# Performance work log

Measured on AMD Instinct MI355X. Metric: run time of the kernel, lower is better.

## Reference

```python
import jax, jax.numpy as jnp
import numpy as np

P, N, E, H = 8192, 32, 256, 8
D = E // H
CUT_A, CUT_B = 0.001, 0.005  # self.length_range = (0.001, 0.005, None, None)
SQRT3 = 1.7320508075688772


def _soft_square_cutoff(x):
    # smooth ramp 0->1 on [CUT_A, CUT_B], 0 below, 1 above (high-side ranges are None)
    t = jnp.clip((x - CUT_A) / (CUT_B - CUT_A), 0.0, 1.0)
    return 0.5 * (1.0 - jnp.cos(jnp.pi * t))


def setup_inputs() -> dict:
    key = jax.random.key(0)
    ks = jax.random.split(key, 16)
    s = 1.0 / np.sqrt(E)
    inp = {
        "query": jax.random.normal(ks[0], (P, E), jnp.float32),
        "key_x": jax.random.normal(ks[1], (P, E), jnp.float32),
        "value": jax.random.normal(ks[2], (P, E), jnp.float32),
        "index_pair": jax.random.randint(ks[3], (P, N), 0, P),
        "relative_atten_weights": jax.random.normal(ks[4], (P, N, H), jnp.float32),
        # lengths ~ N(0, 0.002*sqrt(3)) so they span the (0.001, 0.005) cutoff range
        "rpe_distance": jax.random.normal(ks[5], (P, N, 3), jnp.float32) * 0.002,
        "Wq": jax.random.normal(ks[6], (E, E), jnp.float32) * s,
        "bq": jnp.zeros((E,), jnp.float32),
        "Wk": jax.random.normal(ks[7], (E, E), jnp.float32) * s,
        "bk": jnp.zeros((E,), jnp.float32),
        "Wv": jax.random.normal(ks[8], (E, E), jnp.float32) * s,
        "bv": jnp.zeros((E,), jnp.float32),
        "Wg1": jax.random.normal(ks[9], (E, 3 * H), jnp.float32) * s,
        "bg1": jnp.zeros((3 * H,), jnp.float32),
        "Wg2": jax.random.normal(ks[10], (3 * H, 3 * H), jnp.float32) * (1.0 / np.sqrt(3 * H)),
        "bg2": jnp.zeros((3 * H,), jnp.float32),
    }
    return inp


def reference(query, key_x, value, index_pair, relative_atten_weights, rpe_distance,
              Wq, bq, Wk, bk, Wv, bv, Wg1, bg1, Wg2, bg2):
    # --- RPE spherical harmonics (irreps 1x0e+1x1e, component norm); keep l=1 part ([:,1:])
    rlen = jnp.linalg.norm(rpe_distance, axis=-1, keepdims=True)        # [P,N,1]
    unit = rpe_distance / jnp.maximum(rlen, 1e-12)                      # normalize=True
    cutoff = _soft_square_cutoff(rlen)                                  # nonscalar cutoff
    rpe_edge_sh = SQRT3 * unit * cutoff                                 # [P,N,3]

    # --- projections
    q = query @ Wq + bq                                                 # [P,E]
    k = key_x @ Wk + bk
    v = value @ Wv + bv

    # --- mapper_v6: per-edge gather of key/value rows
    k_g = k[index_pair]                                                 # [P,N,E]
    v_g = v[index_pair]                                                 # [P,N,E]

    # --- dot-product attention logits
    qh = q.reshape(P, H, D)
    kh = k_g.reshape(P, N, H, D)
    dot_atten = jnp.einsum('phd,pnhd->pnh', qh, kh)                     # [P,N,H]

    # --- MLP positional bias gated by spherical harmonics
    diff = k_g - q[:, None, :]                                          # [P,N,E]
    g = jax.nn.relu(diff @ Wg1 + bg1) @ Wg2 + bg2                       # [P,N,3H]
    g = g.reshape(P, N, H, 3)
    pos_atten = jnp.sum(g * rpe_edge_sh[:, :, None, :], axis=-1)        # [P,N,H]

    atten = (dot_atten + pos_atten + relative_atten_weights) / np.sqrt(D)
    atten = jax.nn.softmax(atten, axis=1)                               # over neighbors

    vh = v_g.reshape(P, N, H, D)
    out = jnp.einsum('pnh,pnhc->phc', atten, vh).reshape(P, E)
    return out
```

## Files before the change

kernel.cpp:

```cpp
#include <hip/hip_runtime.h>
#include <stdint.h>

typedef uint32_t u32;
typedef unsigned short u16;

#define LDT 40

typedef __bf16 bf16x8 __attribute__((ext_vector_type(8)));
typedef float  f32x4  __attribute__((ext_vector_type(4)));
typedef _Float16 h16x2 __attribute__((ext_vector_type(2)));
typedef u32    u32x4  __attribute__((ext_vector_type(4)));
typedef u32    u32x2  __attribute__((ext_vector_type(2)));
typedef float  f32x4v __attribute__((ext_vector_type(4)));

__device__ __forceinline__ float bf2f(u16 x) {
  union { float f; u32 u; } c; c.u = ((u32)x) << 16; return c.f;
}
__device__ __forceinline__ u16 f2bf(float f) {
  union { float f; u32 u; } c; c.f = f;
  u32 b = c.u;
  return (u16)((b + 0x7FFFu + ((b >> 16) & 1u)) >> 16);
}
__device__ __forceinline__ u32 pk2(float lo, float hi) {
  return (u32)f2bf(lo) | ((u32)f2bf(hi) << 16);
}
__device__ __forceinline__ u16 f2h(float f) {
  union { _Float16 h; u16 u; } c; c.h = (_Float16)f; return c.u;
}
__device__ __forceinline__ float h2f(u16 x) {
  union { _Float16 h; u16 u; } c; c.u = x; return (float)c.h;
}
__device__ __forceinline__ u32 h2bf2(u32 w) {
  return pk2(h2f((u16)(w & 0xFFFF)), h2f((u16)(w >> 16)));
}
__device__ __forceinline__ float fdot2u(u32 a, u32 b, float c) {
  union { u32 u; h16x2 h; } ua, ub; ua.u = a; ub.u = b;
#if __has_builtin(__builtin_amdgcn_fdot2)
  return __builtin_amdgcn_fdot2(ua.h, ub.h, c, false);
#else
  return c + (float)ua.h.x * (float)ub.h.x + (float)ua.h.y * (float)ub.h.y;
#endif
}

__global__ __launch_bounds__(256) void prep_transpose(
    const float* __restrict__ Wq, const float* __restrict__ Wk, const float* __restrict__ Wv,
    const float* __restrict__ Wg2, const float* __restrict__ Wg1,
    u16* __restrict__ WTq, u16* __restrict__ WTk, u16* __restrict__ WTv,
    u16* __restrict__ wg2bf, u16* __restrict__ wg1T)
{
  int z = blockIdx.z, bx = blockIdx.x, by = blockIdx.y;
  int x = threadIdx.x, y = threadIdx.y;
  if (z == 3) {
    if (bx || by) return;
    int t = y * 32 + x;
    for (int i = t; i < 1280; i += 256) {
      int j = i / 40, k = i % 40;
      float v = (j < 24 && k < 24) ? Wg2[(size_t)k * 24 + j] : 0.f;
      wg2bf[i] = f2bf(v);
    }
    for (int j = 0; j < 24; j++)
      wg1T[(size_t)j * 256 + t] = f2bf(Wg1[(size_t)t * 24 + j]);
    for (int j = 24; j < 32; j++)
      wg1T[(size_t)j * 256 + t] = 0;
    return;
  }
  __shared__ u16 tile[32][33];
  const float* W  = (z == 0) ? Wq : (z == 1) ? Wk : Wv;
  u16*         WT = (z == 0) ? WTq : (z == 1) ? WTk : WTv;
  for (int yy = y; yy < 32; yy += 8)
    tile[yy][x] = f2bf(W[(size_t)(by * 32 + yy) * 256 + bx * 32 + x]);
  __syncthreads();
  for (int yy = y; yy < 32; yy += 8)
    WT[(size_t)(bx * 32 + yy) * 256 + by * 32 + x] = tile[x][yy];
}

__global__ __launch_bounds__(256) void gemm_qkv(
    const float* __restrict__ Xq, const float* __restrict__ Xk, const float* __restrict__ Xv,
    const u16* __restrict__ WTq, const u16* __restrict__ WTk, const u16* __restrict__ WTv,
    const float* __restrict__ bq, const float* __restrict__ bk, const float* __restrict__ bv,
    u16* __restrict__ Oq, u16* __restrict__ Ok, u16* __restrict__ Ov)
{
  int z = blockIdx.z;
  const float* X    = (z == 0) ? Xq : (z == 1) ? Xk : Xv;
  const u16*   WT   = (z == 0) ? WTq : (z == 1) ? WTk : WTv;
  const float* bias = (z == 0) ? bq : (z == 1) ? bk : bv;
  u16*         O    = (z == 0) ? Oq : (z == 1) ? Ok : Ov;

  int m0 = blockIdx.x * 64;
  int n0 = blockIdx.y * 128;
  int t = threadIdx.x;
  int lane = t & 63, wid = t >> 6;
  int wr = wid >> 1, wc = wid & 1;
  int fr = lane & 15, fg = lane >> 4;
  int sra = t >> 2;
  int sca = (t & 3) * 8;
  int srb = t >> 1;
  int scb = (t & 1) * 16;

  __shared__ __align__(16) u16 la[64 * LDT];
  __shared__ __align__(16) u16 lb[128 * LDT];

  f32x4 acc[2][4];
#pragma unroll
  for (int i = 0; i < 2; i++)
#pragma unroll
    for (int j = 0; j < 4; j++) acc[i][j] = (f32x4){0.f, 0.f, 0.f, 0.f};

  for (int kt = 0; kt < 256; kt += 32) {
    const float4* ga = (const float4*)(X + (size_t)(m0 + sra) * 256 + kt + sca);
    float4 a0 = ga[0], a1 = ga[1];
    const uint4* gb = (const uint4*)(WT + (size_t)(n0 + srb) * 256 + kt + scb);
    uint4 b0 = gb[0], b1 = gb[1];

    uint4 wa;
    wa.x = pk2(a0.x, a0.y); wa.y = pk2(a0.z, a0.w);
    wa.z = pk2(a1.x, a1.y); wa.w = pk2(a1.z, a1.w);

    __syncthreads();
    *(uint4*)&la[sra * LDT + sca]     = wa;
    *(uint4*)&lb[srb * LDT + scb]     = b0;
    *(uint4*)&lb[srb * LDT + scb + 8] = b1;
    __syncthreads();

    bf16x8 af[2], bfr[4];
#pragma unroll
    for (int s = 0; s < 2; s++)
      af[s] = *(const bf16x8*)&la[(wr * 32 + s * 16 + fr) * LDT + fg * 8];
#pragma unroll
    for (int j = 0; j < 4; j++)
      bfr[j] = *(const bf16x8*)&lb[(wc * 64 + j * 16 + fr) * LDT + fg * 8];
#pragma unroll
    for (int i = 0; i < 2; i++)
#pragma unroll
      for (int j = 0; j < 4; j++)
        acc[i][j] = __builtin_amdgcn_mfma_f32_16x16x32_bf16(af[i], bfr[j], acc[i][j], 0, 0, 0);
  }

#pragma unroll
  for (int i = 0; i < 2; i++) {
    int rowb = m0 + wr * 32 + i * 16 + fg * 4;
#pragma unroll
    for (int j = 0; j < 4; j++) {
      int col = n0 + wc * 64 + j * 16 + fr;
      float bb = bias[col];
#pragma unroll
      for (int r = 0; r < 4; r++)
        O[(size_t)(rowb + r) * 256 + col] = f2h(acc[i][j][r] + bb);
    }
  }
}

__global__ __launch_bounds__(256) void gemm_g1(
    const u16* __restrict__ kbuf, const u16* __restrict__ qbuf,
    const u16* __restrict__ wg1T, const float* __restrict__ bg1,
    u16* __restrict__ kg1, u16* __restrict__ qadj)
{
  int z = blockIdx.y;
  const u16* X = (z == 0) ? kbuf : qbuf;
  u16*       O = (z == 0) ? kg1 : qadj;

  int m0 = blockIdx.x * 128;
  int t = threadIdx.x;
  int lane = t & 63, wid = t >> 6;
  int fr = lane & 15, fg = lane >> 4;
  int sr = t >> 1;
  int sc = (t & 1) * 16;

  __shared__ __align__(16) u16 la[128 * LDT];
  __shared__ __align__(16) u16 lb[32 * LDT];

  f32x4 acc[2][2];
#pragma unroll
  for (int i = 0; i < 2; i++)
#pragma unroll
    for (int j = 0; j < 2; j++) acc[i][j] = (f32x4){0.f, 0.f, 0.f, 0.f};

  for (int kt = 0; kt < 256; kt += 32) {
    const uint4* ga = (const uint4*)(X + (size_t)(m0 + sr) * 256 + kt + sc);
    uint4 a0 = ga[0], a1 = ga[1];
    uint4 b0, b1;
    if (t < 64) {
      const uint4* gb = (const uint4*)(wg1T + (size_t)sr * 256 + kt + sc);
      b0 = gb[0]; b1 = gb[1];
    }
    uint4 wa0, wa1;
    wa0.x = h2bf2(a0.x); wa0.y = h2bf2(a0.y);
    wa0.z = h2bf2(a0.z); wa0.w = h2bf2(a0.w);
    wa1.x = h2bf2(a1.x); wa1.y = h2bf2(a1.y);
    wa1.z = h2bf2(a1.z); wa1.w = h2bf2(a1.w);

    __syncthreads();
    *(uint4*)&la[sr * LDT + sc]     = wa0;
    *(uint4*)&la[sr * LDT + sc + 8] = wa1;
    if (t < 64) {
      *(uint4*)&lb[sr * LDT + sc]     = b0;
      *(uint4*)&lb[sr * LDT + sc + 8] = b1;
    }
    __syncthreads();

    bf16x8 af[2], bfr[2];
#pragma unroll
    for (int s = 0; s < 2; s++)
      af[s] = *(const bf16x8*)&la[(wid * 32 + s * 16 + fr) * LDT + fg * 8];
#pragma unroll
    for (int s = 0; s < 2; s++)
      bfr[s] = *(const bf16x8*)&lb[(s * 16 + fr) * LDT + fg * 8];
#pragma unroll
    for (int i = 0; i < 2; i++)
#pragma unroll
      for (int j = 0; j < 2; j++)
        acc[i][j] = __builtin_amdgcn_mfma_f32_16x16x32_bf16(af[i], bfr[j], acc[i][j], 0, 0, 0);
  }

#pragma unroll
  for (int i = 0; i < 2; i++) {
    int rowb = m0 + wid * 32 + i * 16 + fg * 4;
#pragma unroll
    for (int j = 0; j < 2; j++) {
      int col = j * 16 + fr;
      if (col < 24) {
        float sub = (z == 1) ? bg1[col] : 0.f;
#pragma unroll
        for (int r = 0; r < 4; r++)
          O[(size_t)(rowb + r) * 32 + col] = f2h(acc[i][j][r] - sub);
      }
    }
  }
}

__global__ __launch_bounds__(256) void attn_logits(
    const u16* __restrict__ qb, const u16* __restrict__ kb,
    const u16* __restrict__ kg1g, const u16* __restrict__ qadjg,
    const int* __restrict__ ip, const float* __restrict__ raw,
    const float* __restrict__ rpe, const u16* __restrict__ wg2bf,
    const float* __restrict__ bg2g, u16* __restrict__ attg)
{
  int p = blockIdx.x, t = threadIdx.x;
  int lane = t & 63, w = t >> 6;
  int fr = lane & 15, fg = lane >> 4;
  int n = t >> 3, h = t & 7;

  __shared__ __align__(16) u16   wg2_s[32 * 40];
  __shared__ __align__(16) u16   kg1_s[32 * 40];
  __shared__              float qadj_s[24];
  __shared__              float bg2_s[24];
  __shared__              float sh_s[96];
  __shared__              float g_s[32 * 33];
  __shared__              float ev_s[256];
  __shared__              float is_s[8];

  int myidx = ip[(size_t)p * 32 + n];

  uint4 kg1w = {0, 0, 0, 0};
  if ((t & 7) < 4) kg1w = *(const uint4*)(kg1g + (size_t)myidx * 32 + (t & 7) * 8);
  uint4 wgw = {0, 0, 0, 0};
  if (t < 160) wgw = ((const uint4*)wg2bf)[t];
  float rx = 0.f, ry = 0.f, rz = 0.f;
  if (t >= 160 && t < 192) {
    int nn = t - 160;
    rx = __builtin_nontemporal_load(rpe + (size_t)p * 96 + nn * 3 + 0);
    ry = __builtin_nontemporal_load(rpe + (size_t)p * 96 + nn * 3 + 1);
    rz = __builtin_nontemporal_load(rpe + (size_t)p * 96 + nn * 3 + 2);
  }
  u16 qaw = 0;
  if (t >= 192 && t < 216)
    qaw = __builtin_nontemporal_load(qadjg + (size_t)p * 32 + (t - 192));
  float bgw = 0.f;
  if (t >= 224 && t < 248) bgw = bg2g[t - 224];

  const uint4* kr = (const uint4*)(kb + (size_t)myidx * 256 + h * 32);
  uint4 k0 = kr[0], k1 = kr[1], k2 = kr[2], k3 = kr[3];
  const u32x4* qr = (const u32x4*)(qb + (size_t)p * 256 + h * 32);
  u32x4 q0 = __builtin_nontemporal_load(qr + 0);
  u32x4 q1 = __builtin_nontemporal_load(qr + 1);
  u32x4 q2 = __builtin_nontemporal_load(qr + 2);
  u32x4 q3 = __builtin_nontemporal_load(qr + 3);
  float rw = __builtin_nontemporal_load(raw + (size_t)p * 256 + t);

  if ((t & 7) < 4) *(uint4*)&kg1_s[n * 40 + (t & 7) * 8] = kg1w;
  if (t < 160) *(uint4*)&wg2_s[t * 8] = wgw;
  else if (t < 192) {
    int nn = t - 160;
    float rl = sqrtf(rx * rx + ry * ry + rz * rz);
    float inv = 1.f / fmaxf(rl, 1e-12f);
    float tt2 = fminf(fmaxf((rl - 0.001f) * 250.f, 0.f), 1.f);
    float cut = 0.5f * (1.f - cosf(tt2 * 3.14159265358979f));
    float s3c = 1.7320508075688772f * inv * cut;
    sh_s[nn * 3 + 0] = rx * s3c; sh_s[nn * 3 + 1] = ry * s3c; sh_s[nn * 3 + 2] = rz * s3c;
  }
  else if (t >= 192 && t < 216) qadj_s[t - 192] = h2f(qaw);
  else if (t >= 224 && t < 248) bg2_s[t - 224] = bgw;
  __syncthreads();

  {
    int mt = w & 1, jt = w >> 1;
    union { u32 u[4]; bf16x8 v; } a;
    if (fg < 3) {
      const u16*   krow = &kg1_s[(mt * 16 + fr) * 40 + fg * 8];
      const float* qrow = &qadj_s[fg * 8];
      float x0 = fmaxf(h2f(krow[0]) - qrow[0], 0.f), x1 = fmaxf(h2f(krow[1]) - qrow[1], 0.f);
      float x2 = fmaxf(h2f(krow[2]) - qrow[2], 0.f), x3 = fmaxf(h2f(krow[3]) - qrow[3], 0.f);
      float x4 = fmaxf(h2f(krow[4]) - qrow[4], 0.f), x5 = fmaxf(h2f(krow[5]) - qrow[5], 0.f);
      float x6 = fmaxf(h2f(krow[6]) - qrow[6], 0.f), x7 = fmaxf(h2f(krow[7]) - qrow[7], 0.f);
      a.u[0] = pk2(x0, x1); a.u[1] = pk2(x2, x3);
      a.u[2] = pk2(x4, x5); a.u[3] = pk2(x6, x7);
    } else {
      a.u[0] = a.u[1] = a.u[2] = a.u[3] = 0;
    }
    bf16x8 b = *(const bf16x8*)&wg2_s[(jt * 16 + fr) * 40 + fg * 8];
    f32x4 g = (f32x4){0.f, 0.f, 0.f, 0.f};
    g = __builtin_amdgcn_mfma_f32_16x16x32_bf16(a.v, b, g, 0, 0, 0);
    int j = jt * 16 + fr;
    float bb = (j < 24) ? bg2_s[j] : 0.f;
    int e0 = mt * 16 + fg * 4;
#pragma unroll
    for (int r = 0; r < 4; r++)
      g_s[(e0 + r) * 33 + j] = g[r] + bb;
  }
  __syncthreads();

  float ev;
  {
    float dot = 0.f;
    dot = fdot2u(k0.x, q0[0], dot); dot = fdot2u(k0.y, q0[1], dot);
    dot = fdot2u(k0.z, q0[2], dot); dot = fdot2u(k0.w, q0[3], dot);
    dot = fdot2u(k1.x, q1[0], dot); dot = fdot2u(k1.y, q1[1], dot);
    dot = fdot2u(k1.z, q1[2], dot); dot = fdot2u(k1.w, q1[3], dot);
    dot = fdot2u(k2.x, q2[0], dot); dot = fdot2u(k2.y, q2[1], dot);
    dot = fdot2u(k2.z, q2[2], dot); dot = fdot2u(k2.w, q2[3], dot);
    dot = fdot2u(k3.x, q3[0], dot); dot = fdot2u(k3.y, q3[1], dot);
    dot = fdot2u(k3.z, q3[2], dot); dot = fdot2u(k3.w, q3[3], dot);
    float pos = g_s[n * 33 + h * 3 + 0] * sh_s[n * 3 + 0]
              + g_s[n * 33 + h * 3 + 1] * sh_s[n * 3 + 1]
              + g_s[n * 33 + h * 3 + 2] * sh_s[n * 3 + 2];
    ev = __expf((dot + pos + rw) * 0.17677669529663687f);
    ev_s[t] = ev;
  }
  __syncthreads();

  if (w == 0) {
    int hh = lane & 7, g4 = lane >> 3;
    float s = ev_s[(g4 * 4 + 0) * 8 + hh] + ev_s[(g4 * 4 + 1) * 8 + hh]
            + ev_s[(g4 * 4 + 2) * 8 + hh] + ev_s[(g4 * 4 + 3) * 8 + hh];
    s += __shfl_xor(s, 8, 64);
    s += __shfl_xor(s, 16, 64);
    s += __shfl_xor(s, 32, 64);
    if (lane < 8) is_s[hh] = 1.f / s;
  }
  __syncthreads();

  __builtin_nontemporal_store(f2h(ev * is_s[h]), attg + (size_t)p * 256 + t);
}

__global__ __launch_bounds__(256) void attn_pv(
    const u16* __restrict__ vb, const u16* __restrict__ attg,
    const int* __restrict__ ip, float* __restrict__ out)
{
  int t = threadIdx.x, wid = t >> 6, l = t & 63;
  int p = blockIdx.x * 4 + wid;
  __shared__ __align__(8) u16 att_s[4][256];
  __shared__ int idx_s[4][32];

  u32x2 aw = __builtin_nontemporal_load((const u32x2*)(attg + (size_t)p * 256 + l * 4));
  *(u32x2*)&att_s[wid][l * 4] = aw;
  if (l < 32) idx_s[wid][l] = ip[(size_t)p * 32 + l];

  int hh = l >> 3;
  float a0 = 0.f, a1 = 0.f, a2 = 0.f, a3 = 0.f;
#pragma unroll
  for (int n = 0; n < 32; n++) {
    float wt = h2f(att_s[wid][n * 8 + hh]);
    uint2 vv = *(const uint2*)(vb + (size_t)idx_s[wid][n] * 256 + l * 4);
    a0 += wt * h2f((u16)(vv.x & 0xFFFF));
    a1 += wt * h2f((u16)(vv.x >> 16));
    a2 += wt * h2f((u16)(vv.y & 0xFFFF));
    a3 += wt * h2f((u16)(vv.y >> 16));
  }
  f32x4v r; r[0] = a0; r[1] = a1; r[2] = a2; r[3] = a3;
  __builtin_nontemporal_store(r, (f32x4v*)(out + (size_t)p * 256 + l * 4));
}

extern "C" void kernel_launch(void* const* d_in, const int* in_sizes, int n_in,
                              void* d_out, int out_size, void* d_ws, size_t ws_size,
                              hipStream_t stream) {
  const float* query = (const float*)d_in[0];
  const float* key_x = (const float*)d_in[1];
  const float* value = (const float*)d_in[2];
  const int*   index_pair = (const int*)d_in[3];
  const float* raw  = (const float*)d_in[4];
  const float* rpe  = (const float*)d_in[5];
  const float* Wq = (const float*)d_in[6];
  const float* bq = (const float*)d_in[7];
  const float* Wk = (const float*)d_in[8];
  const float* bk = (const float*)d_in[9];
  const float* Wv = (const float*)d_in[10];
  const float* bv = (const float*)d_in[11];
  const float* Wg1 = (const float*)d_in[12];
  const float* bg1 = (const float*)d_in[13];
  const float* Wg2 = (const float*)d_in[14];
  const float* bg2 = (const float*)d_in[15];
  float* out = (float*)d_out;

  char* ws = (char*)d_ws;
  u16*   qbuf  = (u16*)(ws);
  u16*   kbuf  = (u16*)(ws + (4u << 20));
  u16*   vbuf  = (u16*)(ws + (8u << 20));
  u16*   attb  = (u16*)(ws + (12u << 20));
  u16*   qadj  = (u16*)(ws + (16u << 20));
  u16*   kg1   = (u16*)(ws + (16u << 20) + 524288);
  u16*   WTq   = (u16*)(ws + (17u << 20));
  u16*   WTk   = WTq + 65536;
  u16*   WTv   = WTk + 65536;
  u16*   wg2bf = WTv + 65536;
  u16*   wg1T  = wg2bf + 1280;

  prep_transpose<<<dim3(8, 8, 4), dim3(32, 8, 1), 0, stream>>>(
      Wq, Wk, Wv, Wg2, Wg1, WTq, WTk, WTv, wg2bf, wg1T);
  gemm_qkv<<<dim3(128, 2, 3), 256, 0, stream>>>(
      query, key_x, value, WTq, WTk, WTv, bq, bk, bv, qbuf, kbuf, vbuf);
  gemm_g1<<<dim3(64, 2), 256, 0, stream>>>(
      kbuf, qbuf, wg1T, bg1, kg1, qadj);
  attn_logits<<<8192, 256, 0, stream>>>(
      qbuf, kbuf, kg1, qadj, index_pair, raw, rpe, wg2bf, bg2, attb);
  attn_pv<<<2048, 256, 0, stream>>>(
      vbuf, attb, index_pair, out);
}
```

Measured before the change: 64.14 us.

## Fuse attention logits and PV aggregation into one kernel

Merges the logits/softmax kernel with the attention-times-value kernel. Each block now also gathers its 32 neighbor V rows into shared memory up front and does the normalization and weighted sum locally. This removes the fp16 attention buffer round-trip through global memory and one kernel launch. In exchange, shared memory per block grows by about 17KB, which may lower occupancy and raise register pressure from the extra in-flight V loads.

Result: slower. 66.46 us (+3.6%).

```diff
diff --git a/kernel.cpp b/kernel.cpp
--- a/kernel.cpp
+++ b/kernel.cpp
@@ -10,8 +10,6 @@
 typedef float  f32x4  __attribute__((ext_vector_type(4)));
 typedef _Float16 h16x2 __attribute__((ext_vector_type(2)));
 typedef u32    u32x4  __attribute__((ext_vector_type(4)));
-typedef u32    u32x2  __attribute__((ext_vector_type(2)));
-typedef float  f32x4v __attribute__((ext_vector_type(4)));
 
 __device__ __forceinline__ float bf2f(u16 x) {
   union { float f; u32 u; } c; c.u = ((u32)x) << 16; return c.f;
@@ -228,18 +226,19 @@
   }
 }
 
-__global__ __launch_bounds__(256) void attn_logits(
-    const u16* __restrict__ qb, const u16* __restrict__ kb,
+__global__ __launch_bounds__(256) void attn_fused(
+    const u16* __restrict__ qb, const u16* __restrict__ kb, const u16* __restrict__ vb,
     const u16* __restrict__ kg1g, const u16* __restrict__ qadjg,
     const int* __restrict__ ip, const float* __restrict__ raw,
     const float* __restrict__ rpe, const u16* __restrict__ wg2bf,
-    const float* __restrict__ bg2g, u16* __restrict__ attg)
+    const float* __restrict__ bg2g, float* __restrict__ out)
 {
   int p = blockIdx.x, t = threadIdx.x;
   int lane = t & 63, w = t >> 6;
   int fr = lane & 15, fg = lane >> 4;
   int n = t >> 3, h = t & 7;
 
+  __shared__ __align__(16) u16   v_s[32 * 264];
   __shared__ __align__(16) u16   wg2_s[32 * 40];
   __shared__ __align__(16) u16   kg1_s[32 * 40];
   __shared__              float qadj_s[24];
@@ -247,12 +246,22 @@
   __shared__              float sh_s[96];
   __shared__              float g_s[32 * 33];
   __shared__              float ev_s[256];
-  __shared__              float is_s[8];
 
   int myidx = ip[(size_t)p * 32 + n];
 
+  int vc0 = (t & 7) * 32;
+  const uint4* vp = (const uint4*)(vb + (size_t)myidx * 256 + vc0);
+  uint4 v0 = vp[0], v1 = vp[1], v2 = vp[2], v3 = vp[3];
   uint4 kg1w = {0, 0, 0, 0};
   if ((t & 7) < 4) kg1w = *(const uint4*)(kg1g + (size_t)myidx * 32 + (t & 7) * 8);
+  const uint4* kr = (const uint4*)(kb + (size_t)myidx * 256 + h * 32);
+  uint4 k0 = kr[0], k1 = kr[1], k2 = kr[2], k3 = kr[3];
+  const u32x4* qr = (const u32x4*)(qb + (size_t)p * 256 + h * 32);
+  u32x4 q0 = __builtin_nontemporal_load(qr + 0);
+  u32x4 q1 = __builtin_nontemporal_load(qr + 1);
+  u32x4 q2 = __builtin_nontemporal_load(qr + 2);
+  u32x4 q3 = __builtin_nontemporal_load(qr + 3);
+  float rw = __builtin_nontemporal_load(raw + (size_t)p * 256 + t);
   uint4 wgw = {0, 0, 0, 0};
   if (t < 160) wgw = ((const uint4*)wg2bf)[t];
   float rx = 0.f, ry = 0.f, rz = 0.f;
@@ -267,15 +276,6 @@
     qaw = __builtin_nontemporal_load(qadjg + (size_t)p * 32 + (t - 192));
   float bgw = 0.f;
   if (t >= 224 && t < 248) bgw = bg2g[t - 224];
-
-  const uint4* kr = (const uint4*)(kb + (size_t)myidx * 256 + h * 32);
-  uint4 k0 = kr[0], k1 = kr[1], k2 = kr[2], k3 = kr[3];
-  const u32x4* qr = (const u32x4*)(qb + (size_t)p * 256 + h * 32);
-  u32x4 q0 = __builtin_nontemporal_load(qr + 0);
-  u32x4 q1 = __builtin_nontemporal_load(qr + 1);
-  u32x4 q2 = __builtin_nontemporal_load(qr + 2);
-  u32x4 q3 = __builtin_nontemporal_load(qr + 3);
-  float rw = __builtin_nontemporal_load(raw + (size_t)p * 256 + t);
 
   if ((t & 7) < 4) *(uint4*)&kg1_s[n * 40 + (t & 7) * 8] = kg1w;
   if (t < 160) *(uint4*)&wg2_s[t * 8] = wgw;
@@ -290,6 +290,11 @@
   }
   else if (t >= 192 && t < 216) qadj_s[t - 192] = h2f(qaw);
   else if (t >= 224 && t < 248) bg2_s[t - 224] = bgw;
+  {
+    u16* d = &v_s[n * 264 + vc0];
+    ((uint4*)d)[0] = v0; *(uint4*)(d + 8) = v1;
+    *(uint4*)(d + 16) = v2; *(uint4*)(d + 24) = v3;
+  }
   __syncthreads();
 
   {
@@ -319,7 +324,6 @@
   }
   __syncthreads();
 
-  float ev;
   {
     float dot = 0.f;
     dot = fdot2u(k0.x, q0[0], dot); dot = fdot2u(k0.y, q0[1], dot);
@@ -333,51 +337,21 @@
     float pos = g_s[n * 33 + h * 3 + 0] * sh_s[n * 3 + 0]
               + g_s[n * 33 + h * 3 + 1] * sh_s[n * 3 + 1]
               + g_s[n * 33 + h * 3 + 2] * sh_s[n * 3 + 2];
-    ev = __expf((dot + pos + rw) * 0.17677669529663687f);
-    ev_s[t] = ev;
+    ev_s[t] = __expf((dot + pos + rw) * 0.17677669529663687f);
   }
   __syncthreads();
 
-  if (w == 0) {
-    int hh = lane & 7, g4 = lane >> 3;
-    float s = ev_s[(g4 * 4 + 0) * 8 + hh] + ev_s[(g4 * 4 + 1) * 8 + hh]
-            + ev_s[(g4 * 4 + 2) * 8 + hh] + ev_s[(g4 * 4 + 3) * 8 + hh];
-    s += __shfl_xor(s, 8, 64);
-    s += __shfl_xor(s, 16, 64);
-    s += __shfl_xor(s, 32, 64);
-    if (lane < 8) is_s[hh] = 1.f / s;
-  }
-  __syncthreads();
-
-  __builtin_nontemporal_store(f2h(ev * is_s[h]), attg + (size_t)p * 256 + t);
-}
-
-__global__ __launch_bounds__(256) void attn_pv(
-    const u16* __restrict__ vb, const u16* __restrict__ attg,
-    const int* __restrict__ ip, float* __restrict__ out)
-{
-  int t = threadIdx.x, wid = t >> 6, l = t & 63;
-  int p = blockIdx.x * 4 + wid;
-  __shared__ __align__(8) u16 att_s[4][256];
-  __shared__ int idx_s[4][32];
-
-  u32x2 aw = __builtin_nontemporal_load((const u32x2*)(attg + (size_t)p * 256 + l * 4));
-  *(u32x2*)&att_s[wid][l * 4] = aw;
-  if (l < 32) idx_s[wid][l] = ip[(size_t)p * 32 + l];
-
-  int hh = l >> 3;
-  float a0 = 0.f, a1 = 0.f, a2 = 0.f, a3 = 0.f;
-#pragma unroll
-  for (int n = 0; n < 32; n++) {
-    float wt = h2f(att_s[wid][n * 8 + hh]);
-    uint2 vv = *(const uint2*)(vb + (size_t)idx_s[wid][n] * 256 + l * 4);
-    a0 += wt * h2f((u16)(vv.x & 0xFFFF));
-    a1 += wt * h2f((u16)(vv.x >> 16));
-    a2 += wt * h2f((u16)(vv.y & 0xFFFF));
-    a3 += wt * h2f((u16)(vv.y >> 16));
-  }
-  f32x4v r; r[0] = a0; r[1] = a1; r[2] = a2; r[3] = a3;
-  __builtin_nontemporal_store(r, (f32x4v*)(out + (size_t)p * 256 + l * 4));
+  {
+    int hh = t >> 5;
+    float s = 0.f, acc = 0.f;
+#pragma unroll
+    for (int nn = 0; nn < 32; nn++) {
+      float evn = ev_s[nn * 8 + hh];
+      s += evn;
+      acc += evn * h2f(v_s[nn * 264 + t]);
+    }
+    __builtin_nontemporal_store(acc / s, out + (size_t)p * 256 + t);
+  }
 }
 
 extern "C" void kernel_launch(void* const* d_in, const int* in_sizes, int n_in,
@@ -405,10 +379,9 @@
   u16*   qbuf  = (u16*)(ws);
   u16*   kbuf  = (u16*)(ws + (4u << 20));
   u16*   vbuf  = (u16*)(ws + (8u << 20));
-  u16*   attb  = (u16*)(ws + (12u << 20));
-  u16*   qadj  = (u16*)(ws + (16u << 20));
-  u16*   kg1   = (u16*)(ws + (16u << 20) + 524288);
-  u16*   WTq   = (u16*)(ws + (17u << 20));
+  u16*   qadj  = (u16*)(ws + (12u << 20));
+  u16*   kg1   = (u16*)(ws + (12u << 20) + 524288);
+  u16*   WTq   = (u16*)(ws + (13u << 20));
   u16*   WTk   = WTq + 65536;
   u16*   WTv   = WTk + 65536;
   u16*   wg2bf = WTv + 65536;
@@ -420,8 +393,6 @@
       query, key_x, value, WTq, WTk, WTv, bq, bk, bv, qbuf, kbuf, vbuf);
   gemm_g1<<<dim3(64, 2), 256, 0, stream>>>(
       kbuf, qbuf, wg1T, bg1, kg1, qadj);
-  attn_logits<<<8192, 256, 0, stream>>>(
-      qbuf, kbuf, kg1, qadj, index_pair, raw, rpe, wg2bf, bg2, attb);
-  attn_pv<<<2048, 256, 0, stream>>>(
-      vbuf, attb, index_pair, out);
-}
+  attn_fused<<<8192, 256, 0, stream>>>(
+      qbuf, kbuf, vbuf, kg1, qadj, index_pair, raw, rpe, wg2bf, bg2, out);
+}
```
